# Optimization experiments

Hardware: AMD Instinct MI355X
Metric: run time of the kernel (lower is better)

The kernel has to match this reference:

```python
import jax, jax.numpy as jnp
import numpy as np

B, N, C, H, SR = 4, 4096, 512, 8, 2
HD = C // H           # head_dim = 64
SCALE = HD ** -0.5
EPS = 1e-5


def setup_inputs() -> dict:
    key = jax.random.key(0)
    ks = jax.random.split(key, 6)
    s = 0.02
    return {
        "x": jax.random.normal(ks[0], (B, N, C), jnp.float32),
        # weights stored [in, out] (transposed vs torch nn.Linear)
        "w_qkv": jax.random.normal(ks[1], (C, 3 * C), jnp.float32) * s,
        "w_proj": jax.random.normal(ks[2], (C, C), jnp.float32) * s,
        "b_proj": jnp.zeros((C,), jnp.float32),
        # depthwise conv: OIHW with I=1, feature_group_count=C
        "w_sr_conv": jax.random.normal(ks[3], (C, 1, SR, SR), jnp.float32) * s,
        "b_sr_conv": jnp.zeros((C,), jnp.float32),
        "sr_norm_scale": jnp.ones((C,), jnp.float32),
        "sr_norm_bias": jnp.zeros((C,), jnp.float32),
        "w_sr_linear": jax.random.normal(ks[4], (C, HD), jnp.float32) * s,
        "b_sr_linear": jnp.zeros((HD,), jnp.float32),
    }


def reference(x, w_qkv, w_proj, b_proj, w_sr_conv, b_sr_conv,
              sr_norm_scale, sr_norm_bias, w_sr_linear, b_sr_linear):
    Bx, Nx, Cx = x.shape
    # qkv projection (no bias), split into heads
    qkv = (x @ w_qkv).reshape(Bx, Nx, 3, H, HD).transpose(2, 0, 3, 1, 4)  # [3,B,H,N,HD]
    q, k, v = qkv[0], qkv[1], qkv[2]

    # spatial-reduction branch (sr_ratio > 1)
    S = int(Nx ** 0.5)
    x_ = x.transpose(0, 2, 1).reshape(Bx, Cx, S, S)
    x_ = jax.lax.conv_general_dilated(
        x_, w_sr_conv, window_strides=(SR, SR), padding='VALID',
        dimension_numbers=('NCHW', 'OIHW', 'NCHW'), feature_group_count=Cx)
    x_ = x_ + b_sr_conv[None, :, None, None]
    x_ = x_.reshape(Bx, Cx, -1).transpose(0, 2, 1)  # [B, M, C], M = (S/SR)^2
    # LayerNorm over C
    mu = jnp.mean(x_, axis=-1, keepdims=True)
    var = jnp.var(x_, axis=-1, keepdims=True)
    x_ = (x_ - mu) * jax.lax.rsqrt(var + EPS) * sr_norm_scale + sr_norm_bias
    x_ = x_ @ w_sr_linear + b_sr_linear  # [B, M, HD]

    # K/V compression: softmax-weighted pooling of k and v by x_ scores
    scores_k = jax.nn.softmax(jnp.einsum('bmd,bhnd->bhmn', x_, k), axis=-1)
    k = jnp.einsum('bhmn,bhnd->bhmd', scores_k, k)  # [B,H,M,HD]
    scores_v = jax.nn.softmax(jnp.einsum('bmd,bhnd->bhmn', x_, v), axis=-1)
    v = jnp.einsum('bhmn,bhnd->bhmd', scores_v, v)  # [B,H,M,HD]

    # standard attention against compressed K/V
    attn = jax.nn.softmax(jnp.einsum('bhnd,bhmd->bhnm', q, k) * SCALE, axis=-1)
    out = jnp.einsum('bhnm,bhmd->bhnd', attn, v)        # [B,H,N,HD]
    out = out.transpose(0, 2, 1, 3).reshape(Bx, Nx, Cx)  # [B,N,C]
    return out @ w_proj + b_proj
```

## Files before the change

### kernel.cpp

```cpp
#include <hip/hip_runtime.h>

typedef float f32x4 __attribute__((ext_vector_type(4)));
typedef short bf16x8 __attribute__((ext_vector_type(8)));
typedef _Float16 f16x8 __attribute__((ext_vector_type(8)));
typedef __fp16 fp16x2 __attribute__((ext_vector_type(2)));

constexpr int kB  = 4;
constexpr int kN  = 4096;
constexpr int kC  = 512;
constexpr int kH  = 8;
constexpr int kHD = 64;
constexpr int kM  = 1024;
constexpr int kC3 = 1536;

__device__ inline unsigned pkh(float a, float b) {
    union { fp16x2 h; unsigned u; } u;
    u.h = __builtin_amdgcn_cvt_pkrtz(a, b);
    return u.u;
}

__device__ inline float fdot2a(unsigned ph, unsigned ones, float acc) {
    asm("v_dot2_f32_f16 %0, %1, %2, %0" : "+v"(acc) : "v"(ph), "v"(ones));
    return acc;
}

__device__ inline void swap32p(unsigned &a, unsigned &b) {
#if __has_builtin(__builtin_amdgcn_permlane32_swap)
    auto r = __builtin_amdgcn_permlane32_swap(a, b, false, false);
    a = r[0]; b = r[1];
#else
    asm volatile("v_permlane32_swap_b32 %0, %1" : "+v"(a), "+v"(b));
#endif
}
__device__ inline void swap16p(unsigned &a, unsigned &b) {
#if __has_builtin(__builtin_amdgcn_permlane16_swap)
    auto r = __builtin_amdgcn_permlane16_swap(a, b, false, false);
    a = r[0]; b = r[1];
#else
    asm volatile("v_permlane16_swap_b32 %0, %1" : "+v"(a), "+v"(b));
#endif
}

__global__ __launch_bounds__(256) void cvt_f16(
    const float* __restrict__ X, _Float16* __restrict__ Y, int n4)
{
    int i = blockIdx.x * 256 + threadIdx.x;
    if (i >= n4) return;
    float4 v = ((const float4*)X)[i];
    union { _Float16 h[4]; short4 s; } u;
    u.h[0] = (_Float16)v.x; u.h[1] = (_Float16)v.y;
    u.h[2] = (_Float16)v.z; u.h[3] = (_Float16)v.w;
    ((short4*)Y)[i] = u.s;
}

__global__ __launch_bounds__(256) void wcvtT16(
    const float* __restrict__ W, int K, int N, _Float16* __restrict__ T16)
{
    __shared__ float T[64][65];
    const int n0 = blockIdx.x * 64, k0 = blockIdx.y * 64;
    const int t = threadIdx.x;
#pragma unroll
    for (int i = 0; i < 4; i++) {
        int c = t + i * 256;
        int row = c >> 4, col4 = (c & 15) * 4;
        *(float4*)&T[row][col4] = *(const float4*)&W[(size_t)(k0 + row) * N + n0 + col4];
    }
    __syncthreads();
#pragma unroll
    for (int i = 0; i < 4; i++) {
        int c = t + i * 256;
        int nrow = c >> 4, kc4 = (c & 15) * 4;
        union { _Float16 h[4]; short4 s; } u;
        u.h[0] = (_Float16)T[kc4 + 0][nrow];
        u.h[1] = (_Float16)T[kc4 + 1][nrow];
        u.h[2] = (_Float16)T[kc4 + 2][nrow];
        u.h[3] = (_Float16)T[kc4 + 3][nrow];
        *(short4*)&T16[(size_t)(n0 + nrow) * K + k0 + kc4] = u.s;
    }
}

__global__ __launch_bounds__(256) void transpose_hd(
    const short* __restrict__ s0, const short* __restrict__ s1,
    short* __restrict__ d0, short* __restrict__ d1, int nTok)
{
    __shared__ short T[64][72];
    const short* src = blockIdx.z == 0 ? s0 : s1;
    short*       dst = blockIdx.z == 0 ? d0 : d1;
    const int n0 = blockIdx.x * 64, bh = blockIdx.y;
    const int t = threadIdx.x;
#pragma unroll
    for (int i = 0; i < 2; i++) {
        int c = t + i * 256;
        int row = c >> 3, j = (c & 7) * 8;
        *(bf16x8*)&T[row][j] = *(const bf16x8*)&src[((size_t)bh * nTok + n0 + row) * 64 + j];
    }
    __syncthreads();
#pragma unroll
    for (int i = 0; i < 2; i++) {
        int c = t + i * 256;
        int drow = c >> 3, j = (c & 7) * 8;
        bf16x8 v;
#pragma unroll
        for (int q = 0; q < 8; q++) v[q] = T[j + q][drow];
        *(bf16x8*)&dst[((size_t)bh * 64 + drow) * nTok + n0 + j] = v;
    }
}

__global__ __launch_bounds__(256) void gemm_f16(
    const _Float16* __restrict__ A, const _Float16* __restrict__ B,
    int Md, int Nd, int Kd, int mode,
    const float* __restrict__ bias, float* __restrict__ Cf,
    _Float16* __restrict__ q, _Float16* __restrict__ k, _Float16* __restrict__ v)
{
    __shared__ _Float16 Ash[128][40], Bsh[128][40];
    const int t = threadIdx.x, lane = t & 63, L = lane & 15, quad = lane >> 4;
    const int wave = t >> 6, wm = wave >> 1, wn = wave & 1;
    const int bm = blockIdx.y * 128, bn = blockIdx.x * 128;

    f32x4 acc[4][4];
#pragma unroll
    for (int i = 0; i < 4; i++)
#pragma unroll
        for (int j = 0; j < 4; j++) acc[i][j] = (f32x4){0.f, 0.f, 0.f, 0.f};

    for (int k0 = 0; k0 < Kd; k0 += 32) {
#pragma unroll
        for (int i = 0; i < 2; i++) {
            int c = t + i * 256;
            int row = c >> 2, j = (c & 3) * 8;
            *(f16x8*)&Ash[row][j] = *(const f16x8*)&A[(size_t)(bm + row) * Kd + k0 + j];
            *(f16x8*)&Bsh[row][j] = *(const f16x8*)&B[(size_t)(bn + row) * Kd + k0 + j];
        }
        __syncthreads();
        f16x8 af[4];
#pragma unroll
        for (int mi = 0; mi < 4; mi++)
            af[mi] = *(const f16x8*)&Ash[wm * 64 + mi * 16 + L][quad * 8];
#pragma unroll
        for (int ni = 0; ni < 4; ni++) {
            f16x8 bf = *(const f16x8*)&Bsh[wn * 64 + ni * 16 + L][quad * 8];
#pragma unroll
            for (int mi = 0; mi < 4; mi++)
                acc[mi][ni] = __builtin_amdgcn_mfma_f32_16x16x32_f16(af[mi], bf, acc[mi][ni], 0, 0, 0);
        }
        __syncthreads();
    }

    if (mode == 0) {
#pragma unroll
        for (int ni = 0; ni < 4; ni++) {
            int col = bn + wn * 64 + ni * 16 + L;
            float bb = bias ? bias[col] : 0.f;
#pragma unroll
            for (int mi = 0; mi < 4; mi++)
#pragma unroll
                for (int r = 0; r < 4; r++) {
                    int row = bm + wm * 64 + mi * 16 + quad * 4 + r;
                    Cf[(size_t)row * Nd + col] = acc[mi][ni][r] + bb;
                }
        }
    } else {
#pragma unroll
        for (int ni = 0; ni < 4; ni++) {
            int col = bn + wn * 64 + ni * 16 + L;
            int s = col >> 9, h = (col >> 6) & 7, d = col & 63;
            _Float16* dst = s == 0 ? q : s == 1 ? k : v;
#pragma unroll
            for (int mi = 0; mi < 4; mi++)
#pragma unroll
                for (int r = 0; r < 4; r++) {
                    int row = bm + wm * 64 + mi * 16 + quad * 4 + r;
                    int b = row >> 12, n = row & 4095;
                    size_t idx = (((size_t)b * 8 + h) * 4096 + n) * 64 + d;
                    dst[idx] = (_Float16)acc[mi][ni][r];
                }
        }
    }
}

__global__ __launch_bounds__(256) void sr_fused(
    const float* __restrict__ x, const float* __restrict__ wconv,
    const float* __restrict__ bconv, const float* __restrict__ gamma,
    const float* __restrict__ beta, const float* __restrict__ wlin,
    const float* __restrict__ blin, _Float16* __restrict__ xsr)
{
    __shared__ float nbuf[512];
    __shared__ float red[8];
    __shared__ float stats[2];
    __shared__ float pbuf[4][64];

    const int m = blockIdx.x, b = blockIdx.y;
    const int oy = m >> 5, ox = m & 31;
    const int t = threadIdx.x;
    const float* xb = x + (size_t)b * kN * kC;

    float vals[2], s = 0.f, sq = 0.f;
#pragma unroll
    for (int i = 0; i < 2; i++) {
        int c = t + i * 256;
        float acc = bconv[c];
#pragma unroll
        for (int dy = 0; dy < 2; dy++)
#pragma unroll
            for (int dx = 0; dx < 2; dx++) {
                int n = (oy * 2 + dy) * 64 + (ox * 2 + dx);
                acc += xb[(size_t)n * kC + c] * wconv[c * 4 + dy * 2 + dx];
            }
        vals[i] = acc;
        s += acc; sq += acc * acc;
    }
#pragma unroll
    for (int off = 32; off > 0; off >>= 1) {
        s  += __shfl_down(s,  off);
        sq += __shfl_down(sq, off);
    }
    if ((t & 63) == 0) { red[t >> 6] = s; red[4 + (t >> 6)] = sq; }
    __syncthreads();
    if (t == 0) {
        float ts = red[0] + red[1] + red[2] + red[3];
        float tq = red[4] + red[5] + red[6] + red[7];
        float mean = ts * (1.f / 512.f);
        float var  = tq * (1.f / 512.f) - mean * mean;
        stats[0] = mean;
        stats[1] = rsqrtf(var + 1e-5f);
    }
    __syncthreads();
    const float mean = stats[0], rstd = stats[1];
#pragma unroll
    for (int i = 0; i < 2; i++) {
        int c = t + i * 256;
        nbuf[c] = (vals[i] - mean) * rstd * gamma[c] + beta[c];
    }
    __syncthreads();
    const int d = t & 63, part = t >> 6;
    float p = 0.f;
    for (int c = part * 128; c < (part + 1) * 128; c++)
        p += nbuf[c] * wlin[c * 64 + d];
    pbuf[part][d] = p;
    __syncthreads();
    if (t < 64) {
        float o = pbuf[0][t] + pbuf[1][t] + pbuf[2][t] + pbuf[3][t] + blin[t];
        xsr[((size_t)b * kM + m) * kHD + t] = (_Float16)o;
    }
}

__global__ __launch_bounds__(256, 5) void flash_mfma(
    const _Float16* __restrict__ Q, long q_bs, long q_hs,
    const _Float16* __restrict__ K0, const _Float16* __restrict__ K1,
    long k_bs, long k_hs,
    const _Float16* __restrict__ VT0, const _Float16* __restrict__ VT1,
    long v_bs, long v_hs, int v_rs,
    _Float16* __restrict__ O,
    long o_bs, long o_hs, long o_rs, int o_cs,
    int nKtot, int nChunks, float scale, float fixedMax, int kvMerge,
    float* __restrict__ Opart, float* __restrict__ MLpart)
{
    __shared__ _Float16 Ks[64][72];
    __shared__ _Float16 VTs[64][72];
    const int t = threadIdx.x, lane = t & 63, L = lane & 15, quad = lane >> 4;
    const int wave = t >> 6;
    const int h = blockIdx.y;
    int b, which, nB;
    if (kvMerge) { b = blockIdx.z >> 1; which = blockIdx.z & 1; nB = gridDim.z >> 1; }
    else         { b = blockIdx.z;      which = 0;              nB = gridDim.z; }
    const int nMblk = gridDim.x / nChunks;
    const int mblk = blockIdx.x / nChunks, chunk = blockIdx.x % nChunks;
    const int m0 = mblk * 128;
    const int nkc = nKtot / nChunks, nbeg = chunk * nkc, nend = nbeg + nkc;
    const float cl2 = scale * 1.44269504089f;
    const float nmc = -fixedMax * 1.44269504089f;
    const unsigned kOnes = 0x3C003C00u;

    const _Float16* K_ = (which ? K1 : K0) + (size_t)b * k_bs + (size_t)h * k_hs;
    const _Float16* V_ = (which ? VT1 : VT0) + (size_t)b * v_bs + (size_t)h * v_hs;

    f16x8 qf[2][2];
#pragma unroll
    for (int s = 0; s < 2; s++) {
        const size_t qrow = (size_t)b * q_bs + (size_t)h * q_hs
                          + (size_t)(m0 + wave * 32 + s * 16 + L) * 64;
        qf[s][0] = *(const f16x8*)&Q[qrow + quad * 8];
        qf[s][1] = *(const f16x8*)&Q[qrow + 32 + quad * 8];
    }

    f32x4 Oacc[2][4];
#pragma unroll
    for (int s = 0; s < 2; s++)
#pragma unroll
        for (int i = 0; i < 4; i++) Oacc[s][i] = (f32x4){0.f, 0.f, 0.f, 0.f};
    float li[2] = {0.f, 0.f};

    const int sr = t >> 3, sj = (t & 7) * 8;
    f16x8 kp0, kp1, vp0, vp1;
    kp0 = *(const f16x8*)&K_[(size_t)(nbeg + sr) * 64 + sj];
    kp1 = *(const f16x8*)&K_[(size_t)(nbeg + sr + 32) * 64 + sj];
    vp0 = *(const f16x8*)&V_[(size_t)sr * v_rs + nbeg + sj];
    vp1 = *(const f16x8*)&V_[(size_t)(sr + 32) * v_rs + nbeg + sj];

    for (int n0 = nbeg; n0 < nend; n0 += 64) {
        *(f16x8*)&Ks[sr][sj]       = kp0;
        *(f16x8*)&Ks[sr + 32][sj]  = kp1;
        *(f16x8*)&VTs[sr][sj]      = vp0;
        *(f16x8*)&VTs[sr + 32][sj] = vp1;
        __syncthreads();

        int nn = (n0 + 64 < nend) ? n0 + 64 : nbeg;
        kp0 = *(const f16x8*)&K_[(size_t)(nn + sr) * 64 + sj];
        kp1 = *(const f16x8*)&K_[(size_t)(nn + sr + 32) * 64 + sj];
        vp0 = *(const f16x8*)&V_[(size_t)sr * v_rs + nn + sj];
        vp1 = *(const f16x8*)&V_[(size_t)(sr + 32) * v_rs + nn + sj];

        unsigned d0[2][4], d1[2][4];
#pragma unroll
        for (int c = 0; c < 4; c++) {
            f16x8 k0 = *(const f16x8*)&Ks[c * 16 + L][quad * 8];
            f16x8 k1 = *(const f16x8*)&Ks[c * 16 + L][32 + quad * 8];
#pragma unroll
            for (int s = 0; s < 2; s++) {
                f32x4 a = (f32x4){0.f, 0.f, 0.f, 0.f};
                a = __builtin_amdgcn_mfma_f32_16x16x32_f16(k0, qf[s][0], a, 0, 0, 0);
                a = __builtin_amdgcn_mfma_f32_16x16x32_f16(k1, qf[s][1], a, 0, 0, 0);
                float p0 = exp2f(fmaf(a[0], cl2, nmc));
                float p1 = exp2f(fmaf(a[1], cl2, nmc));
                float p2 = exp2f(fmaf(a[2], cl2, nmc));
                float p3 = exp2f(fmaf(a[3], cl2, nmc));
                d0[s][c] = pkh(p0, p1);
                d1[s][c] = pkh(p2, p3);
                li[s] = fdot2a(d0[s][c], kOnes, li[s]);
                li[s] = fdot2a(d1[s][c], kOnes, li[s]);
            }
        }

        f16x8 pt[2][2];
#pragma unroll
        for (int s = 0; s < 2; s++)
#pragma unroll
            for (int h2 = 0; h2 < 2; h2++) {
                unsigned a0 = d0[s][h2 * 2], b0 = d0[s][h2 * 2 + 1];
                swap32p(a0, b0); swap16p(a0, b0);
                unsigned a1 = d1[s][h2 * 2], b1 = d1[s][h2 * 2 + 1];
                swap32p(a1, b1); swap16p(a1, b1);
                union { unsigned u[4]; f16x8 v; } U;
                U.u[0] = a0; U.u[1] = a1; U.u[2] = b0; U.u[3] = b1;
                pt[s][h2] = U.v;
            }

#pragma unroll
        for (int h2 = 0; h2 < 2; h2++) {
#pragma unroll
            for (int dch = 0; dch < 4; dch++) {
                f16x8 vt = *(const f16x8*)&VTs[dch * 16 + L][h2 * 32 + quad * 8];
                Oacc[0][dch] = __builtin_amdgcn_mfma_f32_16x16x32_f16(vt, pt[0][h2], Oacc[0][dch], 0, 0, 0);
                Oacc[1][dch] = __builtin_amdgcn_mfma_f32_16x16x32_f16(vt, pt[1][h2], Oacc[1][dch], 0, 0, 0);
            }
        }
        __syncthreads();
    }

    float lt[2];
#pragma unroll
    for (int s = 0; s < 2; s++) {
        float v = li[s];
        v += __shfl_xor(v, 16);
        v += __shfl_xor(v, 32);
        lt[s] = v;
    }

    if (Opart) {
        int pid = (((which * nB + b) * gridDim.y + h) * nMblk + mblk) * nChunks + chunk;
        float* Ob = Opart + (size_t)pid * (128 * 64);
        float* Mb = MLpart + (size_t)pid * 256;
#pragma unroll
        for (int s = 0; s < 2; s++) {
            int mloc = wave * 32 + s * 16 + L;
#pragma unroll
            for (int dch = 0; dch < 4; dch++)
                *(f32x4*)&Ob[mloc * 64 + dch * 16 + quad * 4] = Oacc[s][dch];
            if (quad == 0) { Mb[mloc] = fixedMax; Mb[128 + mloc] = lt[s]; }
        }
    } else {
#pragma unroll
        for (int s = 0; s < 2; s++) {
            float inv = 1.f / lt[s];
            size_t base = (size_t)b * o_bs + (size_t)h * o_hs
                        + (size_t)(m0 + wave * 32 + s * 16 + L) * o_rs;
#pragma unroll
            for (int dch = 0; dch < 4; dch++)
#pragma unroll
                for (int r = 0; r < 4; r++) {
                    int d = dch * 16 + quad * 4 + r;
                    O[base + (size_t)d * o_cs] = (_Float16)(Oacc[s][dch][r] * inv);
                }
        }
    }
}

__global__ __launch_bounds__(256) void flash_combine(
    const float* __restrict__ Opart, const float* __restrict__ MLpart,
    int nMblk, int nChunks, float cl2,
    _Float16* __restrict__ O, long o_bs, long o_hs, long o_rs, int o_cs)
{
    const int t = threadIdx.x;
    const int b = blockIdx.z, h = blockIdx.y;
    const int qm = blockIdx.x * 4 + (t >> 6), d = t & 63;
    const int mblk = qm >> 7, qloc = qm & 127;
    const int pb = ((b * gridDim.y + h) * nMblk + mblk) * nChunks;
    float mf = -INFINITY;
    for (int c = 0; c < nChunks; c++)
        mf = fmaxf(mf, MLpart[(size_t)(pb + c) * 256 + qloc]);
    float num = 0.f, den = 0.f;
    for (int c = 0; c < nChunks; c++) {
        float mc = MLpart[(size_t)(pb + c) * 256 + qloc];
        float lc = MLpart[(size_t)(pb + c) * 256 + 128 + qloc];
        float w = exp2f((mc - mf) * cl2);
        den += lc * w;
        num += Opart[(size_t)(pb + c) * 8192 + qloc * 64 + d] * w;
    }
    size_t addr = (size_t)b * o_bs + (size_t)h * o_hs + (size_t)qm * o_rs + (size_t)d * o_cs;
    O[addr] = (_Float16)(num / den);
}

extern "C" void kernel_launch(void* const* d_in, const int* in_sizes, int n_in,
                              void* d_out, int out_size, void* d_ws, size_t ws_size,
                              hipStream_t stream)
{
    const float* x      = (const float*)d_in[0];
    const float* w_qkv  = (const float*)d_in[1];
    const float* w_proj = (const float*)d_in[2];
    const float* b_proj = (const float*)d_in[3];
    const float* w_conv = (const float*)d_in[4];
    const float* b_conv = (const float*)d_in[5];
    const float* g_ln   = (const float*)d_in[6];
    const float* b_ln   = (const float*)d_in[7];
    const float* w_lin  = (const float*)d_in[8];
    const float* b_lin  = (const float*)d_in[9];
    float* out = (float*)d_out;
    (void)in_sizes; (void)n_in; (void)out_size; (void)ws_size;

    short* p = (short*)d_ws;
    size_t off = 0;
    auto alloc = [&](size_t n) { short* r = p + off; off += n; return r; };

    const size_t TN = (size_t)kB * kH * kN * kHD;
    const size_t TM = (size_t)kB * kH * kM * kHD;

    _Float16* xf16 = (_Float16*)alloc((size_t)kB * kN * kC);
    _Float16* ao   = xf16;

    _Float16* wq16 = (_Float16*)alloc((size_t)kC3 * kC);
    _Float16* wp16 = (_Float16*)alloc((size_t)kC * kC);
    _Float16* qh  = (_Float16*)alloc(TN);
    _Float16* kh  = (_Float16*)alloc(TN);
    _Float16* vh  = (_Float16*)alloc(TN);
    _Float16* kT  = (_Float16*)alloc(TN);
    _Float16* vT  = (_Float16*)alloc(TN);
    _Float16* xsr = (_Float16*)alloc((size_t)kB * kM * kHD);
    _Float16* kc  = (_Float16*)alloc(TM);
    _Float16* vcT = (_Float16*)alloc(TM);
    float* MLpart = (float*)alloc((size_t)2048 * 256 * 2);
    float* Opart  = (float*)alloc((size_t)2048 * 8192 * 2);

    const int NCH = 4;

    cvt_f16<<<(kB * kN * kC / 4 + 255) / 256, 256, 0, stream>>>(
        x, xf16, kB * kN * kC / 4);

    wcvtT16<<<dim3(kC3 / 64, kC / 64), 256, 0, stream>>>(w_qkv, kC, kC3, wq16);
    wcvtT16<<<dim3(kC / 64, kC / 64), 256, 0, stream>>>(w_proj, kC, kC, wp16);

    gemm_f16<<<dim3(kC3 / 128, kB * kN / 128), 256, 0, stream>>>(
        xf16, wq16, kB * kN, kC3, kC, 1, nullptr, nullptr, qh, kh, vh);

    transpose_hd<<<dim3(kN / 64, kB * kH, 2), 256, 0, stream>>>(
        (const short*)kh, (const short*)vh, (short*)kT, (short*)vT, kN);

    sr_fused<<<dim3(kM, kB), 256, 0, stream>>>(
        x, w_conv, b_conv, g_ln, b_ln, w_lin, b_lin, xsr);

    flash_mfma<<<dim3(8 * NCH, kH, kB * 2), 256, 0, stream>>>(
        xsr, (long)kM * kHD, 0L,
        kh, vh, (long)kH * kN * kHD, (long)kN * kHD,
        kT, vT, (long)kH * kHD * kN, (long)kHD * kN, kN,
        nullptr, 0L, 0L, 0L, 0,
        kN, NCH, 1.0f, 6.0f, 1, Opart, MLpart);
    flash_combine<<<dim3(kM / 4, kH, kB), 256, 0, stream>>>(
        Opart, MLpart, 8, NCH, 1.44269504089f,
        kc, (long)kH * kM * kHD, (long)kM * kHD, 64L, 1);
    flash_combine<<<dim3(kM / 4, kH, kB), 256, 0, stream>>>(
        Opart + (size_t)1024 * 8192, MLpart + (size_t)1024 * 256, 8, NCH,
        1.44269504089f,
        vcT, (long)kH * kHD * kM, (long)kHD * kM, 1L, kM);

    flash_mfma<<<dim3(32, kH, kB), 256, 0, stream>>>(
        qh, (long)kH * kN * kHD, (long)kN * kHD,
        kc, kc, (long)kH * kM * kHD, (long)kM * kHD,
        vcT, vcT, (long)kH * kHD * kM, (long)kHD * kM, kM,
        ao, (long)kN * kC, 64L, (long)kC, 1,
        kM, 1, 0.125f, 2.0f, 0, nullptr, nullptr);

    gemm_f16<<<dim3(kC / 128, kB * kN / 128), 256, 0, stream>>>(
        ao, wp16, kB * kN, kC, kC, 0, b_proj, out,
        nullptr, nullptr, nullptr);
}
```

Before: 423.0 us.

## Double-buffer K/V LDS tiles and raise MFMA wave priority in flash kernel

```diff
diff --git a/kernel.cpp b/kernel.cpp
--- a/kernel.cpp
+++ b/kernel.cpp
@@ -244,7 +244,7 @@
     }
 }
 
-__global__ __launch_bounds__(256, 5) void flash_mfma(
+__global__ __launch_bounds__(256, 4) void flash_mfma(
     const _Float16* __restrict__ Q, long q_bs, long q_hs,
     const _Float16* __restrict__ K0, const _Float16* __restrict__ K1,
     long k_bs, long k_hs,
@@ -255,8 +255,8 @@
     int nKtot, int nChunks, float scale, float fixedMax, int kvMerge,
     float* __restrict__ Opart, float* __restrict__ MLpart)
 {
-    __shared__ _Float16 Ks[64][72];
-    __shared__ _Float16 VTs[64][72];
+    __shared__ _Float16 Ks[2][64][72];
+    __shared__ _Float16 VTs[2][64][72];
     const int t = threadIdx.x, lane = t & 63, L = lane & 15, quad = lane >> 4;
     const int wave = t >> 6;
     const int h = blockIdx.y;
@@ -291,35 +291,39 @@
     float li[2] = {0.f, 0.f};
 
     const int sr = t >> 3, sj = (t & 7) * 8;
-    f16x8 kp0, kp1, vp0, vp1;
-    kp0 = *(const f16x8*)&K_[(size_t)(nbeg + sr) * 64 + sj];
-    kp1 = *(const f16x8*)&K_[(size_t)(nbeg + sr + 32) * 64 + sj];
-    vp0 = *(const f16x8*)&V_[(size_t)sr * v_rs + nbeg + sj];
-    vp1 = *(const f16x8*)&V_[(size_t)(sr + 32) * v_rs + nbeg + sj];
-
+
+    {
+        f16x8 a0 = *(const f16x8*)&K_[(size_t)(nbeg + sr) * 64 + sj];
+        f16x8 a1 = *(const f16x8*)&K_[(size_t)(nbeg + sr + 32) * 64 + sj];
+        f16x8 a2 = *(const f16x8*)&V_[(size_t)sr * v_rs + nbeg + sj];
+        f16x8 a3 = *(const f16x8*)&V_[(size_t)(sr + 32) * v_rs + nbeg + sj];
+        *(f16x8*)&Ks[0][sr][sj]       = a0;
+        *(f16x8*)&Ks[0][sr + 32][sj]  = a1;
+        *(f16x8*)&VTs[0][sr][sj]      = a2;
+        *(f16x8*)&VTs[0][sr + 32][sj] = a3;
+    }
+    __syncthreads();
+
+    int cur = 0;
     for (int n0 = nbeg; n0 < nend; n0 += 64) {
-        *(f16x8*)&Ks[sr][sj]       = kp0;
-        *(f16x8*)&Ks[sr + 32][sj]  = kp1;
-        *(f16x8*)&VTs[sr][sj]      = vp0;
-        *(f16x8*)&VTs[sr + 32][sj] = vp1;
-        __syncthreads();
-
         int nn = (n0 + 64 < nend) ? n0 + 64 : nbeg;
-        kp0 = *(const f16x8*)&K_[(size_t)(nn + sr) * 64 + sj];
-        kp1 = *(const f16x8*)&K_[(size_t)(nn + sr + 32) * 64 + sj];
-        vp0 = *(const f16x8*)&V_[(size_t)sr * v_rs + nn + sj];
-        vp1 = *(const f16x8*)&V_[(size_t)(sr + 32) * v_rs + nn + sj];
+        f16x8 kp0 = *(const f16x8*)&K_[(size_t)(nn + sr) * 64 + sj];
+        f16x8 kp1 = *(const f16x8*)&K_[(size_t)(nn + sr + 32) * 64 + sj];
+        f16x8 vp0 = *(const f16x8*)&V_[(size_t)sr * v_rs + nn + sj];
+        f16x8 vp1 = *(const f16x8*)&V_[(size_t)(sr + 32) * v_rs + nn + sj];
 
         unsigned d0[2][4], d1[2][4];
 #pragma unroll
         for (int c = 0; c < 4; c++) {
-            f16x8 k0 = *(const f16x8*)&Ks[c * 16 + L][quad * 8];
-            f16x8 k1 = *(const f16x8*)&Ks[c * 16 + L][32 + quad * 8];
+            f16x8 k0 = *(const f16x8*)&Ks[cur][c * 16 + L][quad * 8];
+            f16x8 k1 = *(const f16x8*)&Ks[cur][c * 16 + L][32 + quad * 8];
 #pragma unroll
             for (int s = 0; s < 2; s++) {
                 f32x4 a = (f32x4){0.f, 0.f, 0.f, 0.f};
+                __builtin_amdgcn_s_setprio(1);
                 a = __builtin_amdgcn_mfma_f32_16x16x32_f16(k0, qf[s][0], a, 0, 0, 0);
                 a = __builtin_amdgcn_mfma_f32_16x16x32_f16(k1, qf[s][1], a, 0, 0, 0);
+                __builtin_amdgcn_s_setprio(0);
                 float p0 = exp2f(fmaf(a[0], cl2, nmc));
                 float p1 = exp2f(fmaf(a[1], cl2, nmc));
                 float p2 = exp2f(fmaf(a[2], cl2, nmc));
@@ -345,16 +349,24 @@
                 pt[s][h2] = U.v;
             }
 
+        __builtin_amdgcn_s_setprio(1);
 #pragma unroll
         for (int h2 = 0; h2 < 2; h2++) {
 #pragma unroll
             for (int dch = 0; dch < 4; dch++) {
-                f16x8 vt = *(const f16x8*)&VTs[dch * 16 + L][h2 * 32 + quad * 8];
+                f16x8 vt = *(const f16x8*)&VTs[cur][dch * 16 + L][h2 * 32 + quad * 8];
                 Oacc[0][dch] = __builtin_amdgcn_mfma_f32_16x16x32_f16(vt, pt[0][h2], Oacc[0][dch], 0, 0, 0);
                 Oacc[1][dch] = __builtin_amdgcn_mfma_f32_16x16x32_f16(vt, pt[1][h2], Oacc[1][dch], 0, 0, 0);
             }
         }
+        __builtin_amdgcn_s_setprio(0);
+
+        *(f16x8*)&Ks[cur ^ 1][sr][sj]       = kp0;
+        *(f16x8*)&Ks[cur ^ 1][sr + 32][sj]  = kp1;
+        *(f16x8*)&VTs[cur ^ 1][sr][sj]      = vp0;
+        *(f16x8*)&VTs[cur ^ 1][sr + 32][sj] = vp1;
         __syncthreads();
+        cur ^= 1;
     }
 
     float lt[2];
```

Measured after the change: 418.2 us. About the same (-1.2%).
